# Performance work log

Measured on AMD Instinct MI355X. Metric: run time of the kernel, lower is better.

## Reference

```python
import jax, jax.numpy as jnp
import numpy as np

LAMBDA = 1.0  # lambda_ from __init__


def _exact_edt(targets):
    """Exact Euclidean distance transform of (1 - targets), i.e. distance from
    each pixel to the nearest pixel where targets == 1. Matches
    scipy.ndimage.distance_transform_edt(1 - targets) per batch sample.
    targets: [B, H, W] int (binary). Returns float32 [B, H, W].
    Separable algorithm:
      G(h, w)   = min_{h': seed(h',w)} |h - h'|        (1D pass along H, via cummax/cummin)
      D(h, w)^2 = min_{w'} (w - w')^2 + G(h, w')^2     (min over columns, broadcast)
    """
    B, H, W = targets.shape
    seed = targets > 0  # [B,H,W]
    h_idx = jnp.arange(H, dtype=jnp.float32)[None, :, None]  # [1,H,1]
    # distance to nearest seed above (running max of seed row-indices)
    last_seed = jax.lax.cummax(jnp.where(seed, h_idx, -jnp.inf), axis=1)
    d_up = h_idx - last_seed
    # distance to nearest seed below (reversed running min of seed row-indices)
    next_seed = jnp.flip(jax.lax.cummin(jnp.flip(jnp.where(seed, h_idx, jnp.inf), 1), axis=1), 1)
    d_dn = next_seed - h_idx
    g2 = jnp.square(jnp.minimum(d_up, d_dn))  # [B,H,W] squared 1D distance (inf if column empty)
    w_idx = jnp.arange(W, dtype=jnp.float32)
    off2 = jnp.square(w_idx[:, None] - w_idx[None, :])  # [W_out, W_in]
    # D2[b,h,wo] = min_wi g2[b,h,wi] + off2[wo,wi]; intermediate [B,H,W,W]
    d2 = jnp.min(g2[:, :, None, :] + off2[None, None, :, :], axis=-1)
    return jnp.sqrt(d2)


def setup_inputs() -> dict:
    key = jax.random.key(0)
    k1, k2 = jax.random.split(key)
    B, H, W = 4, 320, 320
    logits = jax.random.normal(k1, (B, H, W), dtype=jnp.float32)
    targets = jax.random.randint(k2, (B, H, W), 0, 2, dtype=jnp.int32)
    return {"logits": logits, "targets": targets}


def reference(logits, targets):
    probs = jax.nn.sigmoid(logits)
    distance_maps = _exact_edt(targets)  # constant w.r.t. logits (cpu/numpy round-trip in original)
    return (probs * distance_maps).mean() + LAMBDA * (1.0 - probs).mean()
```

## Files before the change

### kernel.cpp

```cpp
#include <hip/hip_runtime.h>
#include <math.h>

#define B_ 4
#define H_ 320
#define W_ 320
#define N_TOTAL (B_ * H_ * W_)
#define ROWS 8
#define HALO 4
#define RSTAGE (ROWS + 2 * HALO)
#define GROUPS (RSTAGE * 5)
#define BLOCKS_PER_B (H_ / ROWS)
#define NBLK (B_ * BLOCKS_PER_B)
#define BLOCK 512
#define FLAG_BASE 0xC0DE0000u

__device__ int fallback_ring_scan(const int* __restrict__ img, int h, int w) {
    int best2 = 0x7fffffff;
    if (img[h * W_ + w] > 0) return 0;
    for (int r = 1; r < H_ + W_; ++r) {
        int r2 = r * r;
        if (r2 >= best2) break;
        int hlo = h - r, hhi = h + r;
        int wlo = w - r, whi = w + r;
        int wl = wlo > 0 ? wlo : 0;
        int wr = whi < (W_ - 1) ? whi : (W_ - 1);
        if (hlo >= 0) {
            const int* rowp = img + hlo * W_;
            for (int ww = wl; ww <= wr; ++ww)
                if (rowp[ww] > 0) { int dw = ww - w; int d2 = r2 + dw * dw; best2 = d2 < best2 ? d2 : best2; }
        }
        if (hhi < H_) {
            const int* rowp = img + hhi * W_;
            for (int ww = wl; ww <= wr; ++ww)
                if (rowp[ww] > 0) { int dw = ww - w; int d2 = r2 + dw * dw; best2 = d2 < best2 ? d2 : best2; }
        }
        int hl = (hlo + 1) > 0 ? (hlo + 1) : 0;
        int hr = (hhi - 1) < (H_ - 1) ? (hhi - 1) : (H_ - 1);
        if (wlo >= 0) {
            for (int hh = hl; hh <= hr; ++hh)
                if (img[hh * W_ + wlo] > 0) { int dh = hh - h; int d2 = dh * dh + r2; best2 = d2 < best2 ? d2 : best2; }
        }
        if (whi < W_) {
            for (int hh = hl; hh <= hr; ++hh)
                if (img[hh * W_ + whi] > 0) { int dh = hh - h; int d2 = dh * dh + r2; best2 = d2 < best2 ? d2 : best2; }
        }
    }
    return best2;
}

__device__ __forceinline__ int nearest_dw(const unsigned long long* __restrict__ row, int w) {
    int s = w + 32;
    int word = s >> 6, sh = s & 63;
    unsigned long long lo = row[word];
    unsigned long long win = sh ? ((lo >> sh) | (row[word + 1] << (64 - sh))) : lo;
    int dw = 64;
    unsigned long long rw = win >> 32;
    unsigned long long lw = win << 32;
    if (rw) dw = __builtin_ctzll(rw);
    if (lw) { int dl = __builtin_clzll(lw) + 1; if (dl < dw) dw = dl; }
    return dw;
}

__global__ __launch_bounds__(BLOCK) void fused_edt_loss(
        const float* __restrict__ logits,
        const int* __restrict__ tgt,
        double* __restrict__ partial ,
        unsigned int* __restrict__ flags ,
        float* __restrict__ out) {
    __shared__ unsigned long long smrow[RSTAGE][8];
    __shared__ double s1[BLOCK / 64], s2[BLOCK / 64];
    __shared__ double own1, own2;

    int bid = blockIdx.x;
    int b = bid / BLOCKS_PER_B;
    int g = bid - b * BLOCKS_PER_B;
    int r0 = g * ROWS;
    const int* __restrict__ img = tgt + b * (H_ * W_);
    int t = threadIdx.x;
    int wv = t >> 6, lane = t & 63;

    if (t < RSTAGE) { smrow[t][0] = 0; smrow[t][6] = 0; smrow[t][7] = 0; }
    for (int gg = wv; gg < GROUPS; gg += BLOCK / 64) {
        int rr = gg / 5, wd = gg - rr * 5;
        int gr = r0 - HALO + rr;
        bool p = false;
        if (gr >= 0 && gr < H_) p = img[gr * W_ + wd * 64 + lane] > 0;
        unsigned long long m = __ballot(p);
        if (lane == 0) smrow[rr][1 + wd] = m;
    }
    __syncthreads();

    int sr = HALO + wv;
    int gh = r0 + wv;
    const float* lrow = logits + (b * H_ + gh) * W_;
    double v1 = 0.0, v2 = 0.0;

    for (int k = 0; k < 5; ++k) {
        int w = lane + (k << 6);
        int dw0 = nearest_dw(smrow[sr], w);
        int best2 = (dw0 < 64) ? dw0 * dw0 : 0x3fffffff;
        for (int dh = 1; dh <= HALO; ++dh) {
            int dh2 = dh * dh;
            if (dh2 >= best2) break;
            int du = nearest_dw(smrow[sr - dh], w);
            if (du < 64) { int c = dh2 + du * du; if (c < best2) best2 = c; }
            int dd = nearest_dw(smrow[sr + dh], w);
            if (dd < 64) { int c = dh2 + dd * dd; if (c < best2) best2 = c; }
        }
        if (best2 > (HALO + 1) * (HALO + 1)) best2 = fallback_ring_scan(img, gh, w);

        float dist = sqrtf((float)best2);
        float x = lrow[w];
        float p = 1.0f / (1.0f + expf(-x));
        v1 += (double)(p * dist);
        v2 += (double)(1.0f - p);
    }

    for (int off = 32; off > 0; off >>= 1) {
        v1 += __shfl_down(v1, off, 64);
        v2 += __shfl_down(v2, off, 64);
    }
    if (lane == 0) { s1[wv] = v1; s2[wv] = v2; }
    __syncthreads();

    if (bid != 0) {
        if (t == 0) {
            double a = s1[0] + s1[1] + s1[2] + s1[3] + s1[4] + s1[5] + s1[6] + s1[7];
            double c = s2[0] + s2[1] + s2[2] + s2[3] + s2[4] + s2[5] + s2[6] + s2[7];
            __hip_atomic_store(&partial[2 * bid], a, __ATOMIC_RELAXED, __HIP_MEMORY_SCOPE_AGENT);
            __hip_atomic_store(&partial[2 * bid + 1], c, __ATOMIC_RELAXED, __HIP_MEMORY_SCOPE_AGENT);
            __hip_atomic_store(&flags[bid], FLAG_BASE | (unsigned)bid,
                               __ATOMIC_RELEASE, __HIP_MEMORY_SCOPE_AGENT);
        }
        return;
    }

    if (t == 0) {
        own1 = s1[0] + s1[1] + s1[2] + s1[3] + s1[4] + s1[5] + s1[6] + s1[7];
        own2 = s2[0] + s2[1] + s2[2] + s2[3] + s2[4] + s2[5] + s2[6] + s2[7];
    }
    __syncthreads();

    double a1 = 0.0, a2 = 0.0;
    if (t >= 1 && t < NBLK) {
        unsigned want = FLAG_BASE | (unsigned)t;
        while (__hip_atomic_load(&flags[t], __ATOMIC_ACQUIRE, __HIP_MEMORY_SCOPE_AGENT) != want) {
            __builtin_amdgcn_s_sleep(1);
        }
        a1 = __hip_atomic_load(&partial[2 * t], __ATOMIC_RELAXED, __HIP_MEMORY_SCOPE_AGENT);
        a2 = __hip_atomic_load(&partial[2 * t + 1], __ATOMIC_RELAXED, __HIP_MEMORY_SCOPE_AGENT);
    }
    for (int off = 32; off > 0; off >>= 1) {
        a1 += __shfl_down(a1, off, 64);
        a2 += __shfl_down(a2, off, 64);
    }
    if (lane == 0) { s1[wv] = a1; s2[wv] = a2; }
    __syncthreads();
    if (t == 0) {
        double ta = own1 + s1[0] + s1[1] + s1[2] + s1[3] + s1[4] + s1[5] + s1[6] + s1[7];
        double tc = own2 + s2[0] + s2[1] + s2[2] + s2[3] + s2[4] + s2[5] + s2[6] + s2[7];
        out[0] = (float)((ta + tc) / (double)N_TOTAL);
    }
}

extern "C" void kernel_launch(void* const* d_in, const int* in_sizes, int n_in,
                              void* d_out, int out_size, void* d_ws, size_t ws_size,
                              hipStream_t stream) {
    const float* logits = (const float*)d_in[0];
    const int* targets  = (const int*)d_in[1];
    float* out = (float*)d_out;
    double* partial = (double*)d_ws;
    unsigned int* flags = (unsigned int*)((char*)d_ws + (size_t)NBLK * 2 * sizeof(double));

    fused_edt_loss<<<NBLK, BLOCK, 0, stream>>>(logits, targets, partial, flags, out);
}
```

Baseline: 64.55 us.

## Split rows across wave halves, prefetch inputs, fold loss into single accumulator

Cuts rows per block from 8 to 5 and uses 10 waves per block, each wave covering half a row. This raises the grid from 160 to 256 blocks so more compute units get work. Logits and target values are loaded into registers before the ballot and barrier, so their memory latency overlaps with staging. The loss is rewritten as 1 + p*(dist-1), which leaves one double accumulator and halves the partial-sum traffic. The cross-block spin-wait still assumes every block is co-resident, which is more demanding with the larger grid and block size.

```diff
diff --git a/kernel.cpp b/kernel.cpp
--- a/kernel.cpp
+++ b/kernel.cpp
@@ -5,13 +5,14 @@
 #define H_ 320
 #define W_ 320
 #define N_TOTAL (B_ * H_ * W_)
-#define ROWS 8
+#define ROWS 5
 #define HALO 4
 #define RSTAGE (ROWS + 2 * HALO)
 #define GROUPS (RSTAGE * 5)
 #define BLOCKS_PER_B (H_ / ROWS)
 #define NBLK (B_ * BLOCKS_PER_B)
-#define BLOCK 512
+#define BLOCK 640
+#define NW (BLOCK / 64)
 #define FLAG_BASE 0xC0DE0000u
 
 __device__ int fallback_ring_scan(const int* __restrict__ img, int h, int w) {
@@ -68,8 +69,7 @@
         unsigned int* __restrict__ flags ,
         float* __restrict__ out) {
     __shared__ unsigned long long smrow[RSTAGE][8];
-    __shared__ double s1[BLOCK / 64], s2[BLOCK / 64];
-    __shared__ double own1, own2;
+    __shared__ double s1[NW];
 
     int bid = blockIdx.x;
     int b = bid / BLOCKS_PER_B;
@@ -78,88 +78,115 @@
     const int* __restrict__ img = tgt + b * (H_ * W_);
     int t = threadIdx.x;
     int wv = t >> 6, lane = t & 63;
+    int half = (wv >= ROWS) ? 1 : 0;
+    int rr = wv - half * ROWS;
+    int gh = r0 + rr;
+    int wbase = half * 160;
+
+    const float* __restrict__ lrow = logits + (b * H_ + gh) * W_;
+    float xs[3];
+#pragma unroll
+    for (int j = 0; j < 3; ++j) {
+        int w = wbase + (j << 6) + lane;
+        xs[j] = lrow[w < W_ ? w : W_ - 1];
+    }
+
+    int gr0 = r0 - HALO;
+    int ngg = (wv < 5) ? 7 : 6;
+    int vals[7];
+#pragma unroll
+    for (int i = 0; i < 7; ++i) {
+        if (i < ngg) {
+            int gg = wv + i * 10;
+            int rr2 = gg / 5, wd = gg - rr2 * 5;
+            int gr = gr0 + rr2;
+            int grc = gr < 0 ? 0 : (gr >= H_ ? H_ - 1 : gr);
+            vals[i] = img[grc * W_ + (wd << 6) + lane];
+        }
+    }
 
     if (t < RSTAGE) { smrow[t][0] = 0; smrow[t][6] = 0; smrow[t][7] = 0; }
-    for (int gg = wv; gg < GROUPS; gg += BLOCK / 64) {
-        int rr = gg / 5, wd = gg - rr * 5;
-        int gr = r0 - HALO + rr;
-        bool p = false;
-        if (gr >= 0 && gr < H_) p = img[gr * W_ + wd * 64 + lane] > 0;
-        unsigned long long m = __ballot(p);
-        if (lane == 0) smrow[rr][1 + wd] = m;
-    }
-    __syncthreads();
-
-    int sr = HALO + wv;
-    int gh = r0 + wv;
-    const float* lrow = logits + (b * H_ + gh) * W_;
-    double v1 = 0.0, v2 = 0.0;
-
-    for (int k = 0; k < 5; ++k) {
-        int w = lane + (k << 6);
-        int dw0 = nearest_dw(smrow[sr], w);
-        int best2 = (dw0 < 64) ? dw0 * dw0 : 0x3fffffff;
-        for (int dh = 1; dh <= HALO; ++dh) {
-            int dh2 = dh * dh;
-            if (dh2 >= best2) break;
-            int du = nearest_dw(smrow[sr - dh], w);
-            if (du < 64) { int c = dh2 + du * du; if (c < best2) best2 = c; }
-            int dd = nearest_dw(smrow[sr + dh], w);
-            if (dd < 64) { int c = dh2 + dd * dd; if (c < best2) best2 = c; }
-        }
-        if (best2 > (HALO + 1) * (HALO + 1)) best2 = fallback_ring_scan(img, gh, w);
-
-        float dist = sqrtf((float)best2);
-        float x = lrow[w];
-        float p = 1.0f / (1.0f + expf(-x));
-        v1 += (double)(p * dist);
-        v2 += (double)(1.0f - p);
-    }
-
-    for (int off = 32; off > 0; off >>= 1) {
-        v1 += __shfl_down(v1, off, 64);
-        v2 += __shfl_down(v2, off, 64);
-    }
-    if (lane == 0) { s1[wv] = v1; s2[wv] = v2; }
+
+#pragma unroll
+    for (int i = 0; i < 7; ++i) {
+        if (i < ngg) {
+            int gg = wv + i * 10;
+            int rr2 = gg / 5, wd = gg - rr2 * 5;
+            int gr = gr0 + rr2;
+            bool p = (gr >= 0) && (gr < H_) && (vals[i] > 0);
+            unsigned long long m = __ballot(p);
+            if (lane == 0) smrow[rr2][1 + wd] = m;
+        }
+    }
+    __syncthreads();
+
+    int sr = HALO + rr;
+    double acc = 0.0;
+#pragma unroll
+    for (int j = 0; j < 3; ++j) {
+        bool act = (j < 2) || (lane < 32);
+        if (act) {
+            int w = wbase + (j << 6) + lane;
+            int dw0 = nearest_dw(smrow[sr], w);
+            int best2 = (dw0 < 64) ? dw0 * dw0 : 0x3fffffff;
+            for (int dh = 1; dh <= HALO; ++dh) {
+                int dh2 = dh * dh;
+                if (dh2 >= best2) break;
+                int du = nearest_dw(smrow[sr - dh], w);
+                if (du < 64) { int c = dh2 + du * du; if (c < best2) best2 = c; }
+                int dd = nearest_dw(smrow[sr + dh], w);
+                if (dd < 64) { int c = dh2 + dd * dd; if (c < best2) best2 = c; }
+            }
+            if (best2 > (HALO + 1) * (HALO + 1)) best2 = fallback_ring_scan(img, gh, w);
+
+            float dist = sqrtf((float)best2);
+            float x = xs[j];
+            float p = 1.0f / (1.0f + expf(-x));
+            acc += (double)(p * (dist - 1.0f));
+        }
+    }
+
+#pragma unroll
+    for (int off = 32; off > 0; off >>= 1) acc += __shfl_down(acc, off, 64);
+    if (lane == 0) s1[wv] = acc;
     __syncthreads();
 
     if (bid != 0) {
         if (t == 0) {
-            double a = s1[0] + s1[1] + s1[2] + s1[3] + s1[4] + s1[5] + s1[6] + s1[7];
-            double c = s2[0] + s2[1] + s2[2] + s2[3] + s2[4] + s2[5] + s2[6] + s2[7];
-            __hip_atomic_store(&partial[2 * bid], a, __ATOMIC_RELAXED, __HIP_MEMORY_SCOPE_AGENT);
-            __hip_atomic_store(&partial[2 * bid + 1], c, __ATOMIC_RELAXED, __HIP_MEMORY_SCOPE_AGENT);
+            double a = 0.0;
+#pragma unroll
+            for (int i = 0; i < NW; ++i) a += s1[i];
+            __hip_atomic_store(&partial[bid], a, __ATOMIC_RELAXED, __HIP_MEMORY_SCOPE_AGENT);
             __hip_atomic_store(&flags[bid], FLAG_BASE | (unsigned)bid,
                                __ATOMIC_RELEASE, __HIP_MEMORY_SCOPE_AGENT);
         }
         return;
     }
 
+    double own = 0.0;
     if (t == 0) {
-        own1 = s1[0] + s1[1] + s1[2] + s1[3] + s1[4] + s1[5] + s1[6] + s1[7];
-        own2 = s2[0] + s2[1] + s2[2] + s2[3] + s2[4] + s2[5] + s2[6] + s2[7];
-    }
-    __syncthreads();
-
-    double a1 = 0.0, a2 = 0.0;
+#pragma unroll
+        for (int i = 0; i < NW; ++i) own += s1[i];
+    }
+    __syncthreads();
+
+    double a1 = 0.0;
     if (t >= 1 && t < NBLK) {
         unsigned want = FLAG_BASE | (unsigned)t;
         while (__hip_atomic_load(&flags[t], __ATOMIC_ACQUIRE, __HIP_MEMORY_SCOPE_AGENT) != want) {
             __builtin_amdgcn_s_sleep(1);
         }
-        a1 = __hip_atomic_load(&partial[2 * t], __ATOMIC_RELAXED, __HIP_MEMORY_SCOPE_AGENT);
-        a2 = __hip_atomic_load(&partial[2 * t + 1], __ATOMIC_RELAXED, __HIP_MEMORY_SCOPE_AGENT);
-    }
-    for (int off = 32; off > 0; off >>= 1) {
-        a1 += __shfl_down(a1, off, 64);
-        a2 += __shfl_down(a2, off, 64);
-    }
-    if (lane == 0) { s1[wv] = a1; s2[wv] = a2; }
+        a1 = __hip_atomic_load(&partial[t], __ATOMIC_RELAXED, __HIP_MEMORY_SCOPE_AGENT);
+    }
+#pragma unroll
+    for (int off = 32; off > 0; off >>= 1) a1 += __shfl_down(a1, off, 64);
+    if (lane == 0) s1[wv] = a1;
     __syncthreads();
     if (t == 0) {
-        double ta = own1 + s1[0] + s1[1] + s1[2] + s1[3] + s1[4] + s1[5] + s1[6] + s1[7];
-        double tc = own2 + s2[0] + s2[1] + s2[2] + s2[3] + s2[4] + s2[5] + s2[6] + s2[7];
-        out[0] = (float)((ta + tc) / (double)N_TOTAL);
+        double total = own;
+#pragma unroll
+        for (int i = 0; i < NW; ++i) total += s1[i];
+        out[0] = (float)(1.0 + total / (double)N_TOTAL);
     }
 }
 
@@ -170,7 +197,7 @@
     const int* targets  = (const int*)d_in[1];
     float* out = (float*)d_out;
     double* partial = (double*)d_ws;
-    unsigned int* flags = (unsigned int*)((char*)d_ws + (size_t)NBLK * 2 * sizeof(double));
+    unsigned int* flags = (unsigned int*)((char*)d_ws + (size_t)NBLK * sizeof(double));
 
     fused_edt_loss<<<NBLK, BLOCK, 0, stream>>>(logits, targets, partial, flags, out);
 }
```

After: 62.05 us. 1.04x faster.
